# Performance work log

Measured on AMD Instinct MI355X. Metric: run time of the kernel, lower is better.

Reference implementation:

```python
import jax, jax.numpy as jnp
import numpy as np

NEG_INF = -1e9  # matches the TF additive-mask constant


def setup_inputs() -> dict:
    key = jax.random.key(0)
    k1, k2, k3 = jax.random.split(key, 3)
    B, Tq, Tk, D = 8, 2048, 2048, 1024
    decoder_outputs = jax.random.normal(k1, (B, Tq, D), dtype=jnp.float32)
    encoder_outputs = jax.random.normal(k2, (B, Tk, D), dtype=jnp.float32)
    encoder_mask = jax.random.randint(k3, (B, Tk), 0, 2, dtype=jnp.int32)
    return {
        "decoder_outputs": decoder_outputs,
        "encoder_outputs": encoder_outputs,
        "encoder_mask": encoder_mask,
    }


def reference(decoder_outputs, encoder_outputs, encoder_mask):
    # score[b, q, k] = <dec[b, q], enc[b, k]>  (no 1/sqrt(d) scaling in original)
    score = jnp.einsum("bqd,bkd->bqk", decoder_outputs, encoder_outputs)
    m = encoder_mask.astype(score.dtype)[:, None, :]  # [B, 1, Tk]
    score = score + (1.0 - m) * NEG_INF
    attention_weights = jax.nn.softmax(score, axis=-1)
    context_vector = jnp.einsum("bqk,bkd->bqd", attention_weights, encoder_outputs)
    return (context_vector, attention_weights)
```

## Files before the change

### kernel.cpp

```cpp
#include <hip/hip_runtime.h>
#include <cstddef>
#include <cstdint>

typedef _Float16 f16x8 __attribute__((ext_vector_type(8)));
typedef _Float16 f16x4 __attribute__((ext_vector_type(4)));
typedef float f32x4 __attribute__((ext_vector_type(4)));

static constexpr int BATCH = 8;
static constexpr int TQ = 2048;
static constexpr int TK = 2048;
static constexpr int DIM = 1024;
static constexpr size_t CTX_ELEMS = (size_t)BATCH * TQ * DIM;

static constexpr int BM = 128, BN = 128, BK = 32;
static constexpr int LDSS = 40;

__device__ __forceinline__ f16x8 cvt8(float4 a, float4 b) {
  f16x8 h;
  h[0] = (_Float16)a.x; h[1] = (_Float16)a.y; h[2] = (_Float16)a.z; h[3] = (_Float16)a.w;
  h[4] = (_Float16)b.x; h[5] = (_Float16)b.y; h[6] = (_Float16)b.z; h[7] = (_Float16)b.w;
  return h;
}

__global__ __launch_bounds__(256) void score_kernel(
    const float* __restrict__ dec, const float* __restrict__ enc,
    float* __restrict__ S) {
  __shared__ _Float16 sA[BM * LDSS];
  __shared__ _Float16 sB[BN * LDSS];

  const int nt = blockIdx.x, mt = blockIdx.y, b = blockIdx.z;
  const int t = threadIdx.x;
  const int lane = t & 63, wave = t >> 6;
  const int wm = wave >> 1, wn = wave & 1;
  const int tm = lane & 15, quad = lane >> 4;

  const float* Abase = dec + ((size_t)b * TQ + mt * BM) * DIM;
  const float* Bbase = enc + ((size_t)b * TK + nt * BN) * DIM;

  f32x4 acc[4][4] = {};

  const int r = t >> 2;
  const int c8 = (t & 3) * 8;

  for (int k0 = 0; k0 < DIM; k0 += BK) {
    float4 a0 = *(const float4*)(Abase + (size_t)r * DIM + k0 + c8);
    float4 a1 = *(const float4*)(Abase + (size_t)r * DIM + k0 + c8 + 4);
    float4 a2 = *(const float4*)(Abase + (size_t)(r + 64) * DIM + k0 + c8);
    float4 a3 = *(const float4*)(Abase + (size_t)(r + 64) * DIM + k0 + c8 + 4);
    float4 b0 = *(const float4*)(Bbase + (size_t)r * DIM + k0 + c8);
    float4 b1 = *(const float4*)(Bbase + (size_t)r * DIM + k0 + c8 + 4);
    float4 b2 = *(const float4*)(Bbase + (size_t)(r + 64) * DIM + k0 + c8);
    float4 b3 = *(const float4*)(Bbase + (size_t)(r + 64) * DIM + k0 + c8 + 4);

    __syncthreads();
    *(f16x8*)&sA[r * LDSS + c8]        = cvt8(a0, a1);
    *(f16x8*)&sA[(r + 64) * LDSS + c8] = cvt8(a2, a3);
    *(f16x8*)&sB[r * LDSS + c8]        = cvt8(b0, b1);
    *(f16x8*)&sB[(r + 64) * LDSS + c8] = cvt8(b2, b3);
    __syncthreads();

    f16x8 aF[4], bF[4];
#pragma unroll
    for (int i = 0; i < 4; i++)
      aF[i] = *(const f16x8*)&sA[(wm * 64 + i * 16 + tm) * LDSS + quad * 8];
#pragma unroll
    for (int j = 0; j < 4; j++)
      bF[j] = *(const f16x8*)&sB[(wn * 64 + j * 16 + tm) * LDSS + quad * 8];

#pragma unroll
    for (int i = 0; i < 4; i++)
#pragma unroll
      for (int j = 0; j < 4; j++)
        acc[i][j] = __builtin_amdgcn_mfma_f32_16x16x32_f16(aF[i], bF[j], acc[i][j], 0, 0, 0);
  }

#pragma unroll
  for (int i = 0; i < 4; i++) {
#pragma unroll
    for (int rr = 0; rr < 4; rr++) {
      size_t rowoff = ((size_t)b * TQ + mt * BM + wm * 64 + i * 16 + quad * 4 + rr) * (size_t)TK;
#pragma unroll
      for (int j = 0; j < 4; j++)
        S[rowoff + nt * BN + wn * 64 + j * 16 + tm] = acc[i][j][rr];
    }
  }
}

__global__ __launch_bounds__(256) void softmax_kernel(
    float* __restrict__ S, const int* __restrict__ mask) {
  const int row = blockIdx.x;
  const int b = row >> 11;
  float* srow = S + (size_t)row * TK;
  const int* mrow = mask + (size_t)b * TK;
  const int t = threadIdx.x;

  float4 s0 = *(const float4*)(srow + t * 8);
  float4 s1 = *(const float4*)(srow + t * 8 + 4);
  int4 m0 = *(const int4*)(mrow + t * 8);
  int4 m1 = *(const int4*)(mrow + t * 8 + 4);

  float v[8] = {s0.x, s0.y, s0.z, s0.w, s1.x, s1.y, s1.z, s1.w};
  const int mm[8] = {m0.x, m0.y, m0.z, m0.w, m1.x, m1.y, m1.z, m1.w};
#pragma unroll
  for (int i = 0; i < 8; i++)
    if (!mm[i]) v[i] += -1e9f;

  float mx = v[0];
#pragma unroll
  for (int i = 1; i < 8; i++) mx = fmaxf(mx, v[i]);
#pragma unroll
  for (int off = 32; off > 0; off >>= 1) mx = fmaxf(mx, __shfl_down(mx, off));

  __shared__ float redm[4];
  __shared__ float reds[4];
  if ((t & 63) == 0) redm[t >> 6] = mx;
  __syncthreads();
  mx = fmaxf(fmaxf(redm[0], redm[1]), fmaxf(redm[2], redm[3]));

  float e[8];
  float lsum = 0.f;
#pragma unroll
  for (int i = 0; i < 8; i++) {
    e[i] = __expf(v[i] - mx);
    lsum += e[i];
  }
#pragma unroll
  for (int off = 32; off > 0; off >>= 1) lsum += __shfl_down(lsum, off);
  if ((t & 63) == 0) reds[t >> 6] = lsum;
  __syncthreads();
  const float inv = 1.0f / (reds[0] + reds[1] + reds[2] + reds[3]);

  float4 o0 = {e[0] * inv, e[1] * inv, e[2] * inv, e[3] * inv};
  float4 o1 = {e[4] * inv, e[5] * inv, e[6] * inv, e[7] * inv};
  *(float4*)(srow + t * 8) = o0;
  *(float4*)(srow + t * 8 + 4) = o1;
}

__global__ __launch_bounds__(256) void ctx_kernel(
    const float* __restrict__ W, const float* __restrict__ enc,
    float* __restrict__ C) {
  __shared__ _Float16 sA[BM * LDSS];
  __shared__ _Float16 sB[BN * LDSS];

  const int nt = blockIdx.x;
  const int mt = blockIdx.y;
  const int b = blockIdx.z;
  const int t = threadIdx.x;
  const int lane = t & 63, wave = t >> 6;
  const int wm = wave >> 1, wn = wave & 1;
  const int tm = lane & 15, quad = lane >> 4;

  const float* Abase = W + ((size_t)b * TQ + mt * BM) * TK;
  const float* Ebase = enc + (size_t)b * TK * DIM + nt * BN;

  f32x4 acc[4][4] = {};

  const int r = t >> 2;
  const int c8 = (t & 3) * 8;
  const int kkB = (t & 7) * 4;
  const int nnB = (t >> 3) * 4;

  for (int k0 = 0; k0 < TK; k0 += BK) {
    float4 a0 = *(const float4*)(Abase + (size_t)r * TK + k0 + c8);
    float4 a1 = *(const float4*)(Abase + (size_t)r * TK + k0 + c8 + 4);
    float4 a2 = *(const float4*)(Abase + (size_t)(r + 64) * TK + k0 + c8);
    float4 a3 = *(const float4*)(Abase + (size_t)(r + 64) * TK + k0 + c8 + 4);
    float4 f[4];
#pragma unroll
    for (int i = 0; i < 4; i++)
      f[i] = *(const float4*)(Ebase + (size_t)(k0 + kkB + i) * DIM + nnB);

    __syncthreads();
    *(f16x8*)&sA[r * LDSS + c8]        = cvt8(a0, a1);
    *(f16x8*)&sA[(r + 64) * LDSS + c8] = cvt8(a2, a3);
#pragma unroll
    for (int c = 0; c < 4; c++) {
      f16x4 h;
      h[0] = (_Float16)((&f[0].x)[c]);
      h[1] = (_Float16)((&f[1].x)[c]);
      h[2] = (_Float16)((&f[2].x)[c]);
      h[3] = (_Float16)((&f[3].x)[c]);
      *(f16x4*)&sB[(nnB + c) * LDSS + kkB] = h;
    }
    __syncthreads();

    f16x8 aF[4], bF[4];
#pragma unroll
    for (int i = 0; i < 4; i++)
      aF[i] = *(const f16x8*)&sA[(wm * 64 + i * 16 + tm) * LDSS + quad * 8];
#pragma unroll
    for (int j = 0; j < 4; j++)
      bF[j] = *(const f16x8*)&sB[(wn * 64 + j * 16 + tm) * LDSS + quad * 8];

#pragma unroll
    for (int i = 0; i < 4; i++)
#pragma unroll
      for (int j = 0; j < 4; j++)
        acc[i][j] = __builtin_amdgcn_mfma_f32_16x16x32_f16(aF[i], bF[j], acc[i][j], 0, 0, 0);
  }

#pragma unroll
  for (int i = 0; i < 4; i++) {
#pragma unroll
    for (int rr = 0; rr < 4; rr++) {
      size_t rowoff = ((size_t)b * TQ + mt * BM + wm * 64 + i * 16 + quad * 4 + rr) * (size_t)DIM;
#pragma unroll
      for (int j = 0; j < 4; j++)
        C[rowoff + nt * BN + wn * 64 + j * 16 + tm] = acc[i][j][rr];
    }
  }
}

extern "C" void kernel_launch(void* const* d_in, const int* in_sizes, int n_in,
                              void* d_out, int out_size, void* d_ws, size_t ws_size,
                              hipStream_t stream) {
  const float* dec = (const float*)d_in[0];
  const float* enc = (const float*)d_in[1];
  const int* mask = (const int*)d_in[2];

  float* ctx = (float*)d_out;
  float* attn = (float*)d_out + CTX_ELEMS;

  dim3 block(256);
  score_kernel<<<dim3(TK / BN, TQ / BM, BATCH), block, 0, stream>>>(dec, enc, attn);
  softmax_kernel<<<dim3(BATCH * TQ), block, 0, stream>>>(attn, mask);
  ctx_kernel<<<dim3(DIM / BN, TQ / BM, BATCH), block, 0, stream>>>(attn, enc, ctx);
}
```

Baseline: 604.9 us.

## Pre-convert operands to fp16 in workspace and use async global-to-LDS GEMMs

Adds pre-pass kernels that convert decoder and encoder outputs to fp16 and write a transposed fp16 copy of the encoder. Softmax now also writes fp16 attention weights. Both GEMMs become one NT kernel that loads tiles straight into LDS with global_load_lds, which halves global read traffic and removes in-loop conversion and the strided transpose loads. The cost is extra kernel launches, workspace traffic for the converted copies, and an unpadded LDS layout that may cause bank conflicts; the old path remains as a fallback when workspace is too small.

```diff
diff --git a/kernel.cpp b/kernel.cpp
--- a/kernel.cpp
+++ b/kernel.cpp
@@ -11,9 +11,19 @@
 static constexpr int TK = 2048;
 static constexpr int DIM = 1024;
 static constexpr size_t CTX_ELEMS = (size_t)BATCH * TQ * DIM;
-
-static constexpr int BM = 128, BN = 128, BK = 32;
-static constexpr int LDSS = 40;
+static constexpr size_t ATT_ELEMS = (size_t)BATCH * TQ * TK;
+
+static constexpr size_t WS_DEC = 0;
+static constexpr size_t WS_ENC = WS_DEC + CTX_ELEMS;
+static constexpr size_t WS_ENCT = WS_ENC + CTX_ELEMS;
+static constexpr size_t WS_W = WS_ENCT + CTX_ELEMS;
+static constexpr size_t WS_NEEDED_BYTES = (WS_W + ATT_ELEMS) * 2;
+
+__device__ __forceinline__ void async16(const void* g, const void* l) {
+  __builtin_amdgcn_global_load_lds(
+      (const __attribute__((address_space(1))) unsigned int*)g,
+      (__attribute__((address_space(3))) unsigned int*)l, 16, 0, 0);
+}
 
 __device__ __forceinline__ f16x8 cvt8(float4 a, float4 b) {
   f16x8 h;
@@ -22,26 +32,183 @@
   return h;
 }
 
-__global__ __launch_bounds__(256) void score_kernel(
+
+__global__ __launch_bounds__(256) void convert_kernel(
+    const float* __restrict__ dec, const float* __restrict__ enc,
+    _Float16* __restrict__ dec16, _Float16* __restrict__ enc16) {
+  const float* src = blockIdx.y ? enc : dec;
+  _Float16* dst = blockIdx.y ? enc16 : dec16;
+  size_t i = ((size_t)blockIdx.x * 256 + threadIdx.x) * 8;
+  float4 a = *(const float4*)(src + i);
+  float4 b = *(const float4*)(src + i + 4);
+  *(f16x8*)(dst + i) = cvt8(a, b);
+}
+
+__global__ __launch_bounds__(256) void transpose_kernel(
+    const float* __restrict__ enc, _Float16* __restrict__ encT) {
+  __shared__ _Float16 sT[64 * 72];
+  const int k0 = blockIdx.x * 64, d0 = blockIdx.y * 64, b = blockIdx.z;
+  const int t = threadIdx.x;
+  const int krow = t >> 2;
+  const int dcol = (t & 3) * 16;
+
+  const float* src = enc + ((size_t)b * TK + k0 + krow) * DIM + d0 + dcol;
+  float4 f0 = *(const float4*)(src);
+  float4 f1 = *(const float4*)(src + 4);
+  float4 f2 = *(const float4*)(src + 8);
+  float4 f3 = *(const float4*)(src + 12);
+  _Float16 h[16];
+#pragma unroll
+  for (int i = 0; i < 4; i++) {
+    h[i]      = (_Float16)((&f0.x)[i]);
+    h[i + 4]  = (_Float16)((&f1.x)[i]);
+    h[i + 8]  = (_Float16)((&f2.x)[i]);
+    h[i + 12] = (_Float16)((&f3.x)[i]);
+  }
+#pragma unroll
+  for (int i = 0; i < 16; i++)
+    sT[(dcol + i) * 72 + krow] = h[i];
+  __syncthreads();
+
+  const int drow = t >> 2;
+  const int kg = (t & 3) * 16;
+  f16x8 v0 = *(const f16x8*)&sT[drow * 72 + kg];
+  f16x8 v1 = *(const f16x8*)&sT[drow * 72 + kg + 8];
+  _Float16* dst = encT + ((size_t)b * DIM + d0 + drow) * TK + k0 + kg;
+  *(f16x8*)dst = v0;
+  *(f16x8*)(dst + 8) = v1;
+}
+
+template <int M, int N, int K>
+__global__ __launch_bounds__(256) void gemm_nt(
+    const _Float16* __restrict__ A, const _Float16* __restrict__ B,
+    float* __restrict__ C) {
+  __shared__ _Float16 sA[128 * 32];
+  __shared__ _Float16 sB[128 * 32];
+
+  const int nt = blockIdx.x, mt = blockIdx.y, b = blockIdx.z;
+  const int t = threadIdx.x;
+  const int lane = t & 63, w = t >> 6;
+  const int wm = w >> 1, wn = w & 1;
+  const int tm = lane & 15, quad = lane >> 4;
+
+  const _Float16* Ab = A + ((size_t)b * M + mt * 128) * K;
+  const _Float16* Bb = B + ((size_t)b * N + nt * 128) * K;
+
+  const int srow = lane >> 2;
+  const int scol = (lane & 3) * 8;
+
+  f32x4 acc[4][4] = {};
+
+  for (int k0 = 0; k0 < K; k0 += 32) {
+    __syncthreads();
+    async16(Ab + (size_t)(w * 32 + srow) * K + k0 + scol, sA + (w * 32) * 32);
+    async16(Ab + (size_t)(w * 32 + 16 + srow) * K + k0 + scol, sA + (w * 32 + 16) * 32);
+    async16(Bb + (size_t)(w * 32 + srow) * K + k0 + scol, sB + (w * 32) * 32);
+    async16(Bb + (size_t)(w * 32 + 16 + srow) * K + k0 + scol, sB + (w * 32 + 16) * 32);
+    __syncthreads();
+
+    f16x8 aF[4], bF[4];
+#pragma unroll
+    for (int i = 0; i < 4; i++)
+      aF[i] = *(const f16x8*)&sA[(wm * 64 + i * 16 + tm) * 32 + quad * 8];
+#pragma unroll
+    for (int j = 0; j < 4; j++)
+      bF[j] = *(const f16x8*)&sB[(wn * 64 + j * 16 + tm) * 32 + quad * 8];
+
+#pragma unroll
+    for (int i = 0; i < 4; i++)
+#pragma unroll
+      for (int j = 0; j < 4; j++)
+        acc[i][j] = __builtin_amdgcn_mfma_f32_16x16x32_f16(aF[i], bF[j], acc[i][j], 0, 0, 0);
+  }
+
+#pragma unroll
+  for (int i = 0; i < 4; i++) {
+#pragma unroll
+    for (int rr = 0; rr < 4; rr++) {
+      size_t rowoff = ((size_t)b * M + mt * 128 + wm * 64 + i * 16 + quad * 4 + rr) * (size_t)N;
+#pragma unroll
+      for (int j = 0; j < 4; j++)
+        C[rowoff + nt * 128 + wn * 64 + j * 16 + tm] = acc[i][j][rr];
+    }
+  }
+}
+
+__global__ __launch_bounds__(256) void softmax_kernel(
+    float* __restrict__ S, const int* __restrict__ mask, _Float16* __restrict__ W16) {
+  const int row = blockIdx.x;
+  const int b = row >> 11;
+  float* srow = S + (size_t)row * TK;
+  const int* mrow = mask + (size_t)b * TK;
+  const int t = threadIdx.x;
+
+  float4 s0 = *(const float4*)(srow + t * 8);
+  float4 s1 = *(const float4*)(srow + t * 8 + 4);
+  int4 m0 = *(const int4*)(mrow + t * 8);
+  int4 m1 = *(const int4*)(mrow + t * 8 + 4);
+
+  float v[8] = {s0.x, s0.y, s0.z, s0.w, s1.x, s1.y, s1.z, s1.w};
+  const int mm[8] = {m0.x, m0.y, m0.z, m0.w, m1.x, m1.y, m1.z, m1.w};
+#pragma unroll
+  for (int i = 0; i < 8; i++)
+    if (!mm[i]) v[i] += -1e9f;
+
+  float mx = v[0];
+#pragma unroll
+  for (int i = 1; i < 8; i++) mx = fmaxf(mx, v[i]);
+#pragma unroll
+  for (int off = 32; off > 0; off >>= 1) mx = fmaxf(mx, __shfl_down(mx, off));
+
+  __shared__ float redm[4];
+  __shared__ float reds[4];
+  if ((t & 63) == 0) redm[t >> 6] = mx;
+  __syncthreads();
+  mx = fmaxf(fmaxf(redm[0], redm[1]), fmaxf(redm[2], redm[3]));
+
+  float e[8];
+  float lsum = 0.f;
+#pragma unroll
+  for (int i = 0; i < 8; i++) {
+    e[i] = __expf(v[i] - mx);
+    lsum += e[i];
+  }
+#pragma unroll
+  for (int off = 32; off > 0; off >>= 1) lsum += __shfl_down(lsum, off);
+  if ((t & 63) == 0) reds[t >> 6] = lsum;
+  __syncthreads();
+  const float inv = 1.0f / (reds[0] + reds[1] + reds[2] + reds[3]);
+
+  float4 o0 = {e[0] * inv, e[1] * inv, e[2] * inv, e[3] * inv};
+  float4 o1 = {e[4] * inv, e[5] * inv, e[6] * inv, e[7] * inv};
+  *(float4*)(srow + t * 8) = o0;
+  *(float4*)(srow + t * 8 + 4) = o1;
+  if (W16) {
+    f16x8 h;
+    h[0] = (_Float16)o0.x; h[1] = (_Float16)o0.y; h[2] = (_Float16)o0.z; h[3] = (_Float16)o0.w;
+    h[4] = (_Float16)o1.x; h[5] = (_Float16)o1.y; h[6] = (_Float16)o1.z; h[7] = (_Float16)o1.w;
+    *(f16x8*)(W16 + (size_t)row * TK + t * 8) = h;
+  }
+}
+
+static constexpr int BM = 128, BN = 128, BK = 32;
+static constexpr int LDSS = 40;
+
+__global__ __launch_bounds__(256) void score_kernel_fb(
     const float* __restrict__ dec, const float* __restrict__ enc,
     float* __restrict__ S) {
   __shared__ _Float16 sA[BM * LDSS];
   __shared__ _Float16 sB[BN * LDSS];
-
   const int nt = blockIdx.x, mt = blockIdx.y, b = blockIdx.z;
   const int t = threadIdx.x;
   const int lane = t & 63, wave = t >> 6;
   const int wm = wave >> 1, wn = wave & 1;
   const int tm = lane & 15, quad = lane >> 4;
-
   const float* Abase = dec + ((size_t)b * TQ + mt * BM) * DIM;
   const float* Bbase = enc + ((size_t)b * TK + nt * BN) * DIM;
-
   f32x4 acc[4][4] = {};
-
   const int r = t >> 2;
   const int c8 = (t & 3) * 8;
-
   for (int k0 = 0; k0 < DIM; k0 += BK) {
     float4 a0 = *(const float4*)(Abase + (size_t)r * DIM + k0 + c8);
     float4 a1 = *(const float4*)(Abase + (size_t)r * DIM + k0 + c8 + 4);
@@ -51,14 +218,12 @@
     float4 b1 = *(const float4*)(Bbase + (size_t)r * DIM + k0 + c8 + 4);
     float4 b2 = *(const float4*)(Bbase + (size_t)(r + 64) * DIM + k0 + c8);
     float4 b3 = *(const float4*)(Bbase + (size_t)(r + 64) * DIM + k0 + c8 + 4);
-
-    __syncthreads();
-    *(f16x8*)&sA[r * LDSS + c8]        = cvt8(a0, a1);
+    __syncthreads();
+    *(f16x8*)&sA[r * LDSS + c8] = cvt8(a0, a1);
     *(f16x8*)&sA[(r + 64) * LDSS + c8] = cvt8(a2, a3);
-    *(f16x8*)&sB[r * LDSS + c8]        = cvt8(b0, b1);
+    *(f16x8*)&sB[r * LDSS + c8] = cvt8(b0, b1);
     *(f16x8*)&sB[(r + 64) * LDSS + c8] = cvt8(b2, b3);
     __syncthreads();
-
     f16x8 aF[4], bF[4];
 #pragma unroll
     for (int i = 0; i < 4; i++)
@@ -66,14 +231,12 @@
 #pragma unroll
     for (int j = 0; j < 4; j++)
       bF[j] = *(const f16x8*)&sB[(wn * 64 + j * 16 + tm) * LDSS + quad * 8];
-
 #pragma unroll
     for (int i = 0; i < 4; i++)
 #pragma unroll
       for (int j = 0; j < 4; j++)
         acc[i][j] = __builtin_amdgcn_mfma_f32_16x16x32_f16(aF[i], bF[j], acc[i][j], 0, 0, 0);
   }
-
 #pragma unroll
   for (int i = 0; i < 4; i++) {
 #pragma unroll
@@ -86,62 +249,11 @@
   }
 }
 
-__global__ __launch_bounds__(256) void softmax_kernel(
-    float* __restrict__ S, const int* __restrict__ mask) {
-  const int row = blockIdx.x;
-  const int b = row >> 11;
-  float* srow = S + (size_t)row * TK;
-  const int* mrow = mask + (size_t)b * TK;
-  const int t = threadIdx.x;
-
-  float4 s0 = *(const float4*)(srow + t * 8);
-  float4 s1 = *(const float4*)(srow + t * 8 + 4);
-  int4 m0 = *(const int4*)(mrow + t * 8);
-  int4 m1 = *(const int4*)(mrow + t * 8 + 4);
-
-  float v[8] = {s0.x, s0.y, s0.z, s0.w, s1.x, s1.y, s1.z, s1.w};
-  const int mm[8] = {m0.x, m0.y, m0.z, m0.w, m1.x, m1.y, m1.z, m1.w};
-#pragma unroll
-  for (int i = 0; i < 8; i++)
-    if (!mm[i]) v[i] += -1e9f;
-
-  float mx = v[0];
-#pragma unroll
-  for (int i = 1; i < 8; i++) mx = fmaxf(mx, v[i]);
-#pragma unroll
-  for (int off = 32; off > 0; off >>= 1) mx = fmaxf(mx, __shfl_down(mx, off));
-
-  __shared__ float redm[4];
-  __shared__ float reds[4];
-  if ((t & 63) == 0) redm[t >> 6] = mx;
-  __syncthreads();
-  mx = fmaxf(fmaxf(redm[0], redm[1]), fmaxf(redm[2], redm[3]));
-
-  float e[8];
-  float lsum = 0.f;
-#pragma unroll
-  for (int i = 0; i < 8; i++) {
-    e[i] = __expf(v[i] - mx);
-    lsum += e[i];
-  }
-#pragma unroll
-  for (int off = 32; off > 0; off >>= 1) lsum += __shfl_down(lsum, off);
-  if ((t & 63) == 0) reds[t >> 6] = lsum;
-  __syncthreads();
-  const float inv = 1.0f / (reds[0] + reds[1] + reds[2] + reds[3]);
-
-  float4 o0 = {e[0] * inv, e[1] * inv, e[2] * inv, e[3] * inv};
-  float4 o1 = {e[4] * inv, e[5] * inv, e[6] * inv, e[7] * inv};
-  *(float4*)(srow + t * 8) = o0;
-  *(float4*)(srow + t * 8 + 4) = o1;
-}
-
-__global__ __launch_bounds__(256) void ctx_kernel(
+__global__ __launch_bounds__(256) void ctx_kernel_fb(
     const float* __restrict__ W, const float* __restrict__ enc,
     float* __restrict__ C) {
   __shared__ _Float16 sA[BM * LDSS];
   __shared__ _Float16 sB[BN * LDSS];
-
   const int nt = blockIdx.x;
   const int mt = blockIdx.y;
   const int b = blockIdx.z;
@@ -149,17 +261,13 @@
   const int lane = t & 63, wave = t >> 6;
   const int wm = wave >> 1, wn = wave & 1;
   const int tm = lane & 15, quad = lane >> 4;
-
   const float* Abase = W + ((size_t)b * TQ + mt * BM) * TK;
   const float* Ebase = enc + (size_t)b * TK * DIM + nt * BN;
-
   f32x4 acc[4][4] = {};
-
   const int r = t >> 2;
   const int c8 = (t & 3) * 8;
   const int kkB = (t & 7) * 4;
   const int nnB = (t >> 3) * 4;
-
   for (int k0 = 0; k0 < TK; k0 += BK) {
     float4 a0 = *(const float4*)(Abase + (size_t)r * TK + k0 + c8);
     float4 a1 = *(const float4*)(Abase + (size_t)r * TK + k0 + c8 + 4);
@@ -169,9 +277,8 @@
 #pragma unroll
     for (int i = 0; i < 4; i++)
       f[i] = *(const float4*)(Ebase + (size_t)(k0 + kkB + i) * DIM + nnB);
-
-    __syncthreads();
-    *(f16x8*)&sA[r * LDSS + c8]        = cvt8(a0, a1);
+    __syncthreads();
+    *(f16x8*)&sA[r * LDSS + c8] = cvt8(a0, a1);
     *(f16x8*)&sA[(r + 64) * LDSS + c8] = cvt8(a2, a3);
 #pragma unroll
     for (int c = 0; c < 4; c++) {
@@ -183,7 +290,6 @@
       *(f16x4*)&sB[(nnB + c) * LDSS + kkB] = h;
     }
     __syncthreads();
-
     f16x8 aF[4], bF[4];
 #pragma unroll
     for (int i = 0; i < 4; i++)
@@ -191,14 +297,12 @@
 #pragma unroll
     for (int j = 0; j < 4; j++)
       bF[j] = *(const f16x8*)&sB[(wn * 64 + j * 16 + tm) * LDSS + quad * 8];
-
 #pragma unroll
     for (int i = 0; i < 4; i++)
 #pragma unroll
       for (int j = 0; j < 4; j++)
         acc[i][j] = __builtin_amdgcn_mfma_f32_16x16x32_f16(aF[i], bF[j], acc[i][j], 0, 0, 0);
   }
-
 #pragma unroll
   for (int i = 0; i < 4; i++) {
 #pragma unroll
@@ -222,7 +326,21 @@
   float* attn = (float*)d_out + CTX_ELEMS;
 
   dim3 block(256);
-  score_kernel<<<dim3(TK / BN, TQ / BM, BATCH), block, 0, stream>>>(dec, enc, attn);
-  softmax_kernel<<<dim3(BATCH * TQ), block, 0, stream>>>(attn, mask);
-  ctx_kernel<<<dim3(DIM / BN, TQ / BM, BATCH), block, 0, stream>>>(attn, enc, ctx);
-}
+
+  if (ws_size >= WS_NEEDED_BYTES) {
+    _Float16* dec16 = (_Float16*)d_ws + WS_DEC;
+    _Float16* enc16 = (_Float16*)d_ws + WS_ENC;
+    _Float16* encT = (_Float16*)d_ws + WS_ENCT;
+    _Float16* W16 = (_Float16*)d_ws + WS_W;
+
+    convert_kernel<<<dim3(CTX_ELEMS / (256 * 8), 2), block, 0, stream>>>(dec, enc, dec16, enc16);
+    transpose_kernel<<<dim3(TK / 64, DIM / 64, BATCH), block, 0, stream>>>(enc, encT);
+    gemm_nt<TQ, TK, DIM><<<dim3(TK / 128, TQ / 128, BATCH), block, 0, stream>>>(dec16, enc16, attn);
+    softmax_kernel<<<dim3(BATCH * TQ), block, 0, stream>>>(attn, mask, W16);
+    gemm_nt<TQ, DIM, TK><<<dim3(DIM / 128, TQ / 128, BATCH), block, 0, stream>>>(W16, encT, ctx);
+  } else {
+    score_kernel_fb<<<dim3(TK / BN, TQ / BM, BATCH), block, 0, stream>>>(dec, enc, attn);
+    softmax_kernel<<<dim3(BATCH * TQ), block, 0, stream>>>(attn, mask, nullptr);
+    ctx_kernel_fb<<<dim3(DIM / BN, TQ / BM, BATCH), block, 0, stream>>>(attn, enc, ctx);
+  }
+}
```

New measurement: 593.9 us. Within noise of the previous version (-1.8%).
